# Optimization experiments

Hardware: AMD Instinct MI355X
Metric: run time of the kernel (lower is better)

## Reference

```python
import jax, jax.numpy as jnp
import numpy as np

C = 256          # in_channels = out_channels per head
H = 4            # heads
NEG_SLOPE = 0.2  # GATConv leaky_relu slope
EPS = 1e-5       # LayerNorm eps
NUM_LAYERS = 2

# fixed 4-node graph: 9 explicit edges + 4 self loops (PyG GATConv default add_self_loops=True)
SRC = jnp.array([1, 1, 2, 2, 3, 3, 1, 2, 3, 0, 1, 2, 3])
DST = jnp.array([2, 3, 1, 3, 1, 2, 0, 0, 0, 0, 1, 2, 3])
ONEHOT = (DST[:, None] == jnp.arange(4)[None, :]).astype(jnp.float32)  # [E=13, N=4]
MASK = ONEHOT.astype(bool)


def gat_layer(x, W, a_src, a_dst, b):
    """PyG GATConv(C, C, heads=4, concat=False), eval mode (no dropout).
    x: [B,4,C]; W: [C, H*C]; a_src/a_dst: [H,C]; b: [C]."""
    B = x.shape[0]
    xp = (x @ W).reshape(B, 4, H, C)                       # [B,4,H,C]
    e_src = jnp.sum(xp * a_src[None, None], axis=-1)       # [B,4,H]
    e_dst = jnp.sum(xp * a_dst[None, None], axis=-1)       # [B,4,H]
    e = jax.nn.leaky_relu(e_src[:, SRC] + e_dst[:, DST], NEG_SLOPE)  # [B,E,H]
    # softmax over incoming edges per destination node (segment softmax, fixed topology)
    m = jnp.max(jnp.where(MASK[None, :, :, None], e[:, :, None, :], -jnp.inf), axis=1)  # [B,4,H]
    ex = jnp.exp(e - m[:, DST])                            # [B,E,H]
    denom = jnp.einsum('beh,ed->bdh', ex, ONEHOT)          # [B,4,H]
    alpha = ex / denom[:, DST]                             # [B,E,H]
    msg = alpha[..., None] * xp[:, SRC]                    # [B,E,H,C]
    out = jnp.einsum('behc,ed->bdhc', msg, ONEHOT)         # [B,4,H,C]
    return out.mean(axis=2) + b                            # concat=False -> head mean, + bias


def layer_norm(x, g, beta):
    mu = jnp.mean(x, axis=-1, keepdims=True)
    var = jnp.mean((x - mu) ** 2, axis=-1, keepdims=True)
    return (x - mu) * jax.lax.rsqrt(var + EPS) * g + beta


def setup_inputs() -> dict:
    key = jax.random.key(0)
    ks = jax.random.split(key, 20)
    B, HW = 32, 64
    inp = {
        'x_ful': jax.random.normal(ks[0], (B, C, HW, HW), jnp.float32),
        'rgb':   jax.random.normal(ks[1], (B, C, HW, HW), jnp.float32),
        'dep':   jax.random.normal(ks[2], (B, C, HW, HW), jnp.float32),
        'tok':   jax.random.normal(ks[3], (1, C), jnp.float32),
    }
    s = 1.0 / np.sqrt(C)
    for i in range(NUM_LAYERS):
        k = jax.random.split(ks[4 + i], 4)
        inp[f'W{i}'] = jax.random.normal(k[0], (C, H * C), jnp.float32) * s
        inp[f'asrc{i}'] = jax.random.normal(k[1], (H, C), jnp.float32) * s
        inp[f'adst{i}'] = jax.random.normal(k[2], (H, C), jnp.float32) * s
        inp[f'b{i}'] = jnp.zeros((C,), jnp.float32)
        inp[f'g{i}'] = jnp.ones((C,), jnp.float32)
        inp[f'beta{i}'] = jnp.zeros((C,), jnp.float32)
    return inp


def reference(x_ful, rgb, dep, tok,
              W0, asrc0, adst0, b0, g0, beta0,
              W1, asrc1, adst1, b1, g1, beta1):
    B = x_ful.shape[0]
    x1 = rgb.mean(axis=(2, 3))    # squeeze_rgb: global avg pool -> [B,C]
    x2 = dep.mean(axis=(2, 3))
    fu = x_ful.mean(axis=(2, 3))
    tokb = jnp.broadcast_to(tok, (B, C))
    nodes = jnp.stack([tokb, fu, x1, x2], axis=1)  # [B,4,C]

    params = [(W0, asrc0, adst0, b0, g0, beta0), (W1, asrc1, adst1, b1, g1, beta1)]
    g = nodes
    for (W, a_s, a_d, b, gam, bet) in params:
        g = gat_layer(g, W, a_s, a_d, b) + g   # residual
        g = layer_norm(g, gam, bet)
        g = jax.nn.relu(g)

    att = jax.nn.sigmoid(g[:, 0, :])[:, :, None, None]  # token node gates channels
    return x_ful * att + x_ful
```

## Files before the change

### kernel.cpp

```cpp
#include <hip/hip_runtime.h>
#include <hip/hip_bf16.h>

#define CCH 256

typedef float f4 __attribute__((ext_vector_type(4)));

__global__ __launch_bounds__(256, 2) void pool_kernel(
    const float* __restrict__ rgb, const float* __restrict__ dep,
    const float* __restrict__ xf, float* __restrict__ nodes )
{
    const int rw   = blockIdx.x * 4 + (threadIdx.x >> 6);
    const int lane = threadIdx.x & 63;
    const int tensor = rw >> 13;
    const int row    = rw & 8191;
    const float* base = (tensor == 0) ? rgb : (tensor == 1) ? dep : xf;
    const f4* src = (const f4*)(base + (size_t)row * 4096);

    f4 v[16];
#pragma unroll
    for (int j = 0; j < 16; ++j) v[j] = src[lane + 64 * j];
    f4 a0 = v[0] + v[1], a1 = v[2] + v[3], a2 = v[4] + v[5], a3 = v[6] + v[7];
    f4 a4 = v[8] + v[9], a5 = v[10] + v[11], a6 = v[12] + v[13], a7 = v[14] + v[15];
    f4 acc = ((a0 + a1) + (a2 + a3)) + ((a4 + a5) + (a6 + a7));

    float s = acc.x + acc.y + acc.z + acc.w;
#pragma unroll
    for (int off = 32; off; off >>= 1) s += __shfl_down(s, off, 64);
    if (lane == 0) {
        const int b = row >> 8, c = row & 255;
        const int nrow = (tensor == 2) ? 1 : (2 + tensor);
        nodes[(size_t)b * 1024 + nrow * CCH + c] = s * (1.f / 4096.f);
    }
}

__global__ __launch_bounds__(1024) void gatL0_kernel(
    const float* __restrict__ nodes, const float* __restrict__ tok,
    const float* __restrict__ W0, const float* __restrict__ as0,
    const float* __restrict__ ad0, float* __restrict__ msg1)
{
    const int bid = blockIdx.x, b = bid >> 2, h = bid & 3;
    const int t = threadIdx.x, c = t & 255, kq = t >> 8;
    const int lane = t & 63, wv = t >> 6;

    __shared__ float X[4][CCH];
    __shared__ float xpart[3][4][CCH];
    __shared__ float redl[4][8];
    __shared__ float esed[8];
    __shared__ float alpha[4][4];

    X[kq][c] = (kq == 0) ? tok[c] : nodes[(size_t)b * 1024 + kq * 256 + c];
    __syncthreads();

    float acc[4] = {0.f, 0.f, 0.f, 0.f};
    const float* Wp = W0 + h * 256 + c;
    const int kb0 = kq * 64;
    for (int kb = 0; kb < 64; kb += 16) {
        float wr[16];
#pragma unroll
        for (int u = 0; u < 16; ++u) wr[u] = Wp[(size_t)(kb0 + kb + u) * 1024];
#pragma unroll
        for (int u = 0; u < 16; ++u) {
            const int k = kb0 + kb + u;
            float w = wr[u];
            acc[0] += X[0][k] * w;
            acc[1] += X[1][k] * w;
            acc[2] += X[2][k] * w;
            acc[3] += X[3][k] * w;
        }
    }
    if (kq) {
#pragma unroll
        for (int n = 0; n < 4; ++n) xpart[kq - 1][n][c] = acc[n];
    }
    __syncthreads();

    if (kq == 0) {
#pragma unroll
        for (int n = 0; n < 4; ++n)
            acc[n] += xpart[0][n][c] + xpart[1][n][c] + xpart[2][n][c];

        const float av = as0[h * 256 + c], dv = ad0[h * 256 + c];
        float rv[8];
#pragma unroll
        for (int n = 0; n < 4; ++n) { rv[n] = acc[n] * av; rv[4 + n] = acc[n] * dv; }
#pragma unroll
        for (int i = 0; i < 8; ++i)
#pragma unroll
            for (int off = 32; off; off >>= 1)
                rv[i] += __shfl_down(rv[i], off, 64);
        if (lane == 0) {
#pragma unroll
            for (int i = 0; i < 8; ++i) redl[wv][i] = rv[i];
        }
    }
    __syncthreads();
    if (t < 8) esed[t] = redl[0][t] + redl[1][t] + redl[2][t] + redl[3][t];
    __syncthreads();

    if (t < 4) {
        const int cnt[4]     = {4, 3, 3, 3};
        const int srcs[4][4] = {{1,2,3,0},{2,3,1,0},{1,3,2,0},{1,2,3,0}};
        const int d = t, n = cnt[d];
        float v[4], m = -1e30f;
        for (int s = 0; s < n; ++s) {
            float e = esed[srcs[d][s]] + esed[4 + d];
            e = (e >= 0.f) ? e : 0.2f * e;
            v[s] = e; m = fmaxf(m, e);
        }
        float den = 0.f;
        for (int s = 0; s < n; ++s) { v[s] = __expf(v[s] - m); den += v[s]; }
        float inv = 1.f / den;
        for (int s = 0; s < n; ++s) alpha[d][s] = v[s] * inv;
        for (int s = n; s < 4; ++s) alpha[d][s] = 0.f;
    }
    __syncthreads();

    if (kq == 0) {
        const int srcs2[4][4] = {{1,2,3,0},{2,3,1,0},{1,3,2,0},{1,2,3,0}};
#pragma unroll
        for (int d = 0; d < 4; ++d) {
            float s = 0.f;
#pragma unroll
            for (int sl = 0; sl < 4; ++sl)
                s += alpha[d][sl] * acc[srcs2[d][sl]];
            msg1[(size_t)b * 4096 + h * 1024 + d * 256 + c] = s;
        }
    }
}

__global__ __launch_bounds__(1024) void gatL1_kernel(
    const float* __restrict__ nodes, const float* __restrict__ tok,
    const float* __restrict__ msg1,
    const float* __restrict__ b0, const float* __restrict__ g0,
    const float* __restrict__ be0,
    const float* __restrict__ W1, const float* __restrict__ as1,
    const float* __restrict__ ad1, float* __restrict__ msg2tok)
{
    const int bid = blockIdx.x, b = bid >> 2, h = bid & 3;
    const int t = threadIdx.x, c = t & 255, kq = t >> 8;
    const int lane = t & 63, wv = t >> 6;

    __shared__ float X[4][CCH];
    __shared__ float xpart[3][4][CCH];
    __shared__ float redln[16][2];
    __shared__ float mu_s[4], rstd_s[4];
    __shared__ float redl[4][8];
    __shared__ float esed[8];
    __shared__ float alpha[4][4];

    {
        const float* m1 = msg1 + (size_t)b * 4096 + kq * 256 + c;
        float s = m1[0] + m1[1024] + m1[2048] + m1[3072];
        float x0 = (kq == 0) ? tok[c] : nodes[(size_t)b * 1024 + kq * 256 + c];
        float gv = 0.25f * s + b0[c] + x0;
        float ss = gv, qq = gv * gv;
#pragma unroll
        for (int off = 32; off; off >>= 1) {
            ss += __shfl_down(ss, off, 64);
            qq += __shfl_down(qq, off, 64);
        }
        if (lane == 0) { redln[wv][0] = ss; redln[wv][1] = qq; }
        __syncthreads();
        if (t < 4) {
            float s4 = redln[4*t][0] + redln[4*t+1][0] + redln[4*t+2][0] + redln[4*t+3][0];
            float q4 = redln[4*t][1] + redln[4*t+1][1] + redln[4*t+2][1] + redln[4*t+3][1];
            float mu  = s4 * (1.f / 256.f);
            float var = q4 * (1.f / 256.f) - mu * mu;
            mu_s[t] = mu; rstd_s[t] = rsqrtf(var + 1e-5f);
        }
        __syncthreads();
        X[kq][c] = fmaxf((gv - mu_s[kq]) * rstd_s[kq] * g0[c] + be0[c], 0.f);
    }
    __syncthreads();

    float acc[4] = {0.f, 0.f, 0.f, 0.f};
    const float* Wp = W1 + h * 256 + c;
    const int kb0 = kq * 64;
    for (int kb = 0; kb < 64; kb += 16) {
        float wr[16];
#pragma unroll
        for (int u = 0; u < 16; ++u) wr[u] = Wp[(size_t)(kb0 + kb + u) * 1024];
#pragma unroll
        for (int u = 0; u < 16; ++u) {
            const int k = kb0 + kb + u;
            float w = wr[u];
            acc[0] += X[0][k] * w;
            acc[1] += X[1][k] * w;
            acc[2] += X[2][k] * w;
            acc[3] += X[3][k] * w;
        }
    }
    if (kq) {
#pragma unroll
        for (int n = 0; n < 4; ++n) xpart[kq - 1][n][c] = acc[n];
    }
    __syncthreads();

    if (kq == 0) {
#pragma unroll
        for (int n = 0; n < 4; ++n)
            acc[n] += xpart[0][n][c] + xpart[1][n][c] + xpart[2][n][c];

        const float av = as1[h * 256 + c], dv = ad1[h * 256 + c];
        float rv[8];
#pragma unroll
        for (int n = 0; n < 4; ++n) { rv[n] = acc[n] * av; rv[4 + n] = acc[n] * dv; }
#pragma unroll
        for (int i = 0; i < 8; ++i)
#pragma unroll
            for (int off = 32; off; off >>= 1)
                rv[i] += __shfl_down(rv[i], off, 64);
        if (lane == 0) {
#pragma unroll
            for (int i = 0; i < 8; ++i) redl[wv][i] = rv[i];
        }
    }
    __syncthreads();
    if (t < 8) esed[t] = redl[0][t] + redl[1][t] + redl[2][t] + redl[3][t];
    __syncthreads();

    if (t == 0) {
        const int srcs0[4] = {1, 2, 3, 0};
        float v[4], m = -1e30f;
        for (int s = 0; s < 4; ++s) {
            float e = esed[srcs0[s]] + esed[4];
            e = (e >= 0.f) ? e : 0.2f * e;
            v[s] = e; m = fmaxf(m, e);
        }
        float den = 0.f;
        for (int s = 0; s < 4; ++s) { v[s] = __expf(v[s] - m); den += v[s]; }
        float inv = 1.f / den;
        for (int s = 0; s < 4; ++s) alpha[0][s] = v[s] * inv;
    }
    __syncthreads();

    if (kq == 0) {
        const int srcs0[4] = {1, 2, 3, 0};
        float s = 0.f;
#pragma unroll
        for (int sl = 0; sl < 4; ++sl)
            s += alpha[0][sl] * acc[srcs0[sl]];
        msg2tok[(size_t)b * 1024 + h * 256 + c] = s;
    }
}

__global__ __launch_bounds__(256) void finish_kernel(
    const float* __restrict__ tok,
    const float* __restrict__ msg1, const float* __restrict__ msg2tok,
    const float* __restrict__ b0, const float* __restrict__ g0,
    const float* __restrict__ be0,
    const float* __restrict__ b1, const float* __restrict__ g1,
    const float* __restrict__ be1,
    float* __restrict__ scale)
{
    const int b = blockIdx.x, c = threadIdx.x;
    const int lane = c & 63, wv = c >> 6;
    __shared__ float redl[4][2];
    __shared__ float mrs[2];

    const float* m1 = msg1 + (size_t)b * 4096 + c;
    float gv1 = 0.25f * (m1[0] + m1[1024] + m1[2048] + m1[3072]) + b0[c] + tok[c];
    {
        float s = gv1, q = gv1 * gv1;
#pragma unroll
        for (int off = 32; off; off >>= 1) { s += __shfl_down(s, off, 64); q += __shfl_down(q, off, 64); }
        if (lane == 0) { redl[wv][0] = s; redl[wv][1] = q; }
        __syncthreads();
        if (c == 0) {
            float ss = redl[0][0] + redl[1][0] + redl[2][0] + redl[3][0];
            float qq = redl[0][1] + redl[1][1] + redl[2][1] + redl[3][1];
            float mu = ss * (1.f / 256.f);
            mrs[0] = mu; mrs[1] = rsqrtf(qq * (1.f / 256.f) - mu * mu + 1e-5f);
        }
        __syncthreads();
    }
    float y1 = fmaxf((gv1 - mrs[0]) * mrs[1] * g0[c] + be0[c], 0.f);
    __syncthreads();

    const float* m2 = msg2tok + (size_t)b * 1024 + c;
    float gv2 = 0.25f * (m2[0] + m2[256] + m2[512] + m2[768]) + b1[c] + y1;
    {
        float s = gv2, q = gv2 * gv2;
#pragma unroll
        for (int off = 32; off; off >>= 1) { s += __shfl_down(s, off, 64); q += __shfl_down(q, off, 64); }
        if (lane == 0) { redl[wv][0] = s; redl[wv][1] = q; }
        __syncthreads();
        if (c == 0) {
            float ss = redl[0][0] + redl[1][0] + redl[2][0] + redl[3][0];
            float qq = redl[0][1] + redl[1][1] + redl[2][1] + redl[3][1];
            float mu = ss * (1.f / 256.f);
            mrs[0] = mu; mrs[1] = rsqrtf(qq * (1.f / 256.f) - mu * mu + 1e-5f);
        }
        __syncthreads();
    }
    float y2 = fmaxf((gv2 - mrs[0]) * mrs[1] * g1[c] + be1[c], 0.f);
    scale[(size_t)b * CCH + c] = 1.f + 1.f / (1.f + __expf(-y2));
}

__global__ __launch_bounds__(256) void apply_kernel(
    const float* __restrict__ xf, const float* __restrict__ scale,
    float* __restrict__ out, int total4)
{
    int idx = blockIdx.x * 256 + threadIdx.x;
    const int stride = gridDim.x * 256;
    const f4* in4 = (const f4*)xf;
    f4* out4 = (f4*)out;
    for (; idx < total4; idx += stride) {
        f4 v = in4[idx];
        const float s = scale[idx >> 10];
        f4 o = v * s;
        __builtin_nontemporal_store(o, out4 + idx);
    }
}

extern "C" void kernel_launch(void* const* d_in, const int* in_sizes, int n_in,
                              void* d_out, int out_size, void* d_ws, size_t ws_size,
                              hipStream_t stream) {
    const float* x_ful = (const float*)d_in[0];
    const float* rgb   = (const float*)d_in[1];
    const float* dep   = (const float*)d_in[2];
    const float* tok   = (const float*)d_in[3];
    const float* W0  = (const float*)d_in[4];
    const float* as0 = (const float*)d_in[5];
    const float* ad0 = (const float*)d_in[6];
    const float* b0  = (const float*)d_in[7];
    const float* g0  = (const float*)d_in[8];
    const float* be0 = (const float*)d_in[9];
    const float* W1  = (const float*)d_in[10];
    const float* as1 = (const float*)d_in[11];
    const float* ad1 = (const float*)d_in[12];
    const float* b1  = (const float*)d_in[13];
    const float* g1  = (const float*)d_in[14];
    const float* be1 = (const float*)d_in[15];

    float* ws      = (float*)d_ws;
    float* nodes   = ws;
    float* scale   = ws + 32768;
    float* msg1    = ws + 40960;
    float* msg2tok = ws + 172032;
    float* out     = (float*)d_out;

    pool_kernel<<<6144, 256, 0, stream>>>(rgb, dep, x_ful, nodes);
    gatL0_kernel<<<128, 1024, 0, stream>>>(nodes, tok, W0, as0, ad0, msg1);
    gatL1_kernel<<<128, 1024, 0, stream>>>(nodes, tok, msg1, b0, g0, be0,
                                           W1, as1, ad1, msg2tok);
    finish_kernel<<<32, 256, 0, stream>>>(tok, msg1, msg2tok,
                                          b0, g0, be0, b1, g1, be1, scale);
    const int total4 = 32 * CCH * 64 * 64 / 4;
    apply_kernel<<<2048, 256, 0, stream>>>(x_ful, scale, out, total4);
}
```

Baseline: 136.9 us.

## Pool one row per block and use nontemporal loads for rgb/dep

The pooling kernel now gives each block a single 4096-element row, with each of its four waves reducing a quarter through a small shared-memory step, instead of one row per wave with 16 loads in flight. This makes the grid four times larger and lowers register pressure per thread. Reads of rgb and dep, which are never reused, are marked nontemporal so they do not evict x_ful, which the apply kernel reads later. In exchange each block issues fewer loads and adds a __syncthreads and extra block-scheduling overhead.

Result: faster. 133.0 us (-2.9%).

```diff
diff --git a/kernel.cpp b/kernel.cpp
--- a/kernel.cpp
+++ b/kernel.cpp
@@ -5,31 +5,40 @@
 
 typedef float f4 __attribute__((ext_vector_type(4)));
 
-__global__ __launch_bounds__(256, 2) void pool_kernel(
+__global__ __launch_bounds__(256) void pool_kernel(
     const float* __restrict__ rgb, const float* __restrict__ dep,
     const float* __restrict__ xf, float* __restrict__ nodes )
 {
-    const int rw   = blockIdx.x * 4 + (threadIdx.x >> 6);
-    const int lane = threadIdx.x & 63;
-    const int tensor = rw >> 13;
-    const int row    = rw & 8191;
+    const int bid = blockIdx.x;
+    const int t = threadIdx.x;
+    const int lane = t & 63, wv = t >> 6;
+    const int tensor = bid >> 13;
+    const int row    = bid & 8191;
     const float* base = (tensor == 0) ? rgb : (tensor == 1) ? dep : xf;
     const f4* src = (const f4*)(base + (size_t)row * 4096);
 
-    f4 v[16];
-#pragma unroll
-    for (int j = 0; j < 16; ++j) v[j] = src[lane + 64 * j];
-    f4 a0 = v[0] + v[1], a1 = v[2] + v[3], a2 = v[4] + v[5], a3 = v[6] + v[7];
-    f4 a4 = v[8] + v[9], a5 = v[10] + v[11], a6 = v[12] + v[13], a7 = v[14] + v[15];
-    f4 acc = ((a0 + a1) + (a2 + a3)) + ((a4 + a5) + (a6 + a7));
-
-    float s = acc.x + acc.y + acc.z + acc.w;
+    f4 v0, v1, v2, v3;
+    if (tensor < 2) {
+        v0 = __builtin_nontemporal_load(src + t);
+        v1 = __builtin_nontemporal_load(src + t + 256);
+        v2 = __builtin_nontemporal_load(src + t + 512);
+        v3 = __builtin_nontemporal_load(src + t + 768);
+    } else {
+        v0 = src[t]; v1 = src[t + 256]; v2 = src[t + 512]; v3 = src[t + 768];
+    }
+    f4 a = (v0 + v1) + (v2 + v3);
+    float s = a.x + a.y + a.z + a.w;
 #pragma unroll
     for (int off = 32; off; off >>= 1) s += __shfl_down(s, off, 64);
-    if (lane == 0) {
+
+    __shared__ float red[4];
+    if (lane == 0) red[wv] = s;
+    __syncthreads();
+    if (t == 0) {
         const int b = row >> 8, c = row & 255;
         const int nrow = (tensor == 2) ? 1 : (2 + tensor);
-        nodes[(size_t)b * 1024 + nrow * CCH + c] = s * (1.f / 4096.f);
+        nodes[(size_t)b * 1024 + nrow * CCH + c] =
+            (red[0] + red[1] + red[2] + red[3]) * (1.f / 4096.f);
     }
 }
 
@@ -340,7 +349,7 @@
     float* msg2tok = ws + 172032;
     float* out     = (float*)d_out;
 
-    pool_kernel<<<6144, 256, 0, stream>>>(rgb, dep, x_ful, nodes);
+    pool_kernel<<<24576, 256, 0, stream>>>(rgb, dep, x_ful, nodes);
     gatL0_kernel<<<128, 1024, 0, stream>>>(nodes, tok, W0, as0, ad0, msg1);
     gatL1_kernel<<<128, 1024, 0, stream>>>(nodes, tok, msg1, b0, g0, be0,
                                            W1, as1, ad1, msg2tok);
```
